# Optimization experiments

Measured on AMD Instinct MI355X. Metric: run time of the kernel, lower is better.

## Reference

```python
import jax, jax.numpy as jnp
import numpy as np

EPS = 1e-5

def channel_norm(x):
    # per-(batch,channel) norm over spatial dims; torch.var default is unbiased (ddof=1)
    mn = x.mean(axis=(-1, -2), keepdims=True)
    std = jnp.sqrt(x.var(axis=(-1, -2), keepdims=True, ddof=1) + EPS)
    return (x - mn) / std

def conv1x1(x, W, b):
    # x: [B,C,H,W], W: [O,C], b: [O]
    return jnp.einsum('oc,bchw->bohw', W, x) + b[None, :, None, None]

def setup_inputs() -> dict:
    key = jax.random.key(0)
    ks = jax.random.split(key, 10)
    B, C, H, W = 4, 512, 64, 64
    s = 1.0 / np.sqrt(C)  # kaiming-uniform-ish scale for 1x1 conv
    inp = {
        'f_c': jax.random.normal(ks[0], (B, C, H, W), jnp.float32),
        'f_s': jax.random.normal(ks[1], (B, C, H, W), jnp.float32),
        'W_c1': jax.random.uniform(ks[2], (C, C), jnp.float32, -s, s),
        'b_c1': jax.random.uniform(ks[3], (C,), jnp.float32, -s, s),
        'W_s1': jax.random.uniform(ks[4], (C, C), jnp.float32, -s, s),
        'b_s1': jax.random.uniform(ks[5], (C,), jnp.float32, -s, s),
        'W_s2': jax.random.uniform(ks[6], (C, C), jnp.float32, -s, s),
        'b_s2': jax.random.uniform(ks[7], (C,), jnp.float32, -s, s),
        'W_csc': jax.random.uniform(ks[8], (C, C), jnp.float32, -s, s),
        'b_csc': jax.random.uniform(ks[9], (C,), jnp.float32, -s, s),
    }
    return inp

def reference(f_c, f_s, W_c1, b_c1, W_s1, b_s1, W_s2, b_s2, W_csc, b_csc):
    B, C, H, W = f_c.shape
    f_c_hat = channel_norm(f_c)
    f_s_hat = channel_norm(f_s)
    f = conv1x1(f_c_hat, W_c1, b_c1).reshape(B, C, H * W)  # queries [B,C,N]
    g = conv1x1(f_s_hat, W_s1, b_s1).reshape(B, C, H * W)  # keys    [B,C,N]
    scores = jnp.einsum('bci,bcj->bij', f, g)              # [B,N,N]
    attention = jax.nn.softmax(scores, axis=-1)
    h = conv1x1(f_s_hat, W_s2, b_s2).reshape(B, C, H * W)  # values  [B,C,N]
    out = jnp.einsum('bcj,bij->bci', h, attention).reshape(B, C, H, W)
    return conv1x1(out, W_csc, b_csc) + f_c
```

## Files before the change

### kernel.cpp

```cpp
#include <hip/hip_runtime.h>

typedef unsigned short u16;
typedef __attribute__((ext_vector_type(8))) _Float16 f16x8;
typedef __attribute__((ext_vector_type(4))) float f32x4;

#define N_SP 4096
#define C_CH 512
#define B_SZ 4

struct PtrTab { u16* p[4]; };

__device__ __forceinline__ u16 f2h(float f) {
    _Float16 h = (_Float16)f;
    union { _Float16 h; u16 u; } x; x.h = h; return x.u;
}
__device__ __forceinline__ float h2f(u16 u) {
    union { u16 u; _Float16 h; } x; x.u = u; return (float)x.h;
}
__device__ __forceinline__ void async_cp16(const void* g, void* l) {
    __builtin_amdgcn_global_load_lds((const __attribute__((address_space(1))) unsigned*)g,
                                     (__attribute__((address_space(3))) unsigned*)l, 16, 0, 0);
}

__device__ __forceinline__ float wave_reduce_sum(float v) {
    #pragma unroll
    for (int off = 32; off; off >>= 1) v += __shfl_xor(v, off, 64);
    return v;
}
__device__ __forceinline__ float wave_reduce_max(float v) {
    #pragma unroll
    for (int off = 32; off; off >>= 1) v = fmaxf(v, __shfl_xor(v, off, 64));
    return v;
}

__global__ __launch_bounds__(256) void stats_kernel(const float* __restrict__ fc,
                                                    const float* __restrict__ fs,
                                                    float* __restrict__ stats) {
    const int idx = blockIdx.x;
    const float* src = (idx < 2048 ? fc : fs) + (size_t)(idx & 2047) * N_SP;
    const int t = threadIdx.x;
    float s = 0.f, ss = 0.f;
    #pragma unroll
    for (int i = 0; i < 4; ++i) {
        float4 v = *(const float4*)(src + i * 1024 + t * 4);
        s  += v.x + v.y + v.z + v.w;
        ss += v.x * v.x + v.y * v.y + v.z * v.z + v.w * v.w;
    }
    s = wave_reduce_sum(s); ss = wave_reduce_sum(ss);
    __shared__ float rs[4], rss[4];
    const int wave = t >> 6;
    if ((t & 63) == 0) { rs[wave] = s; rss[wave] = ss; }
    __syncthreads();
    if (t == 0) {
        const float S  = rs[0] + rs[1] + rs[2] + rs[3];
        const float SS = rss[0] + rss[1] + rss[2] + rss[3];
        const float mean = S * (1.f / N_SP);
        const float var  = (SS - S * mean) * (1.f / (N_SP - 1));
        stats[idx * 2 + 0] = mean;
        stats[idx * 2 + 1] = rsqrtf(var + 1e-5f);
    }
}

__global__ __launch_bounds__(256) void norm_transpose(
        const float* __restrict__ fc, const float* __restrict__ fs,
        const float* __restrict__ stats,
        u16* __restrict__ xc, u16* __restrict__ xs) {
    __shared__ float tile[64][65];
    __shared__ float mi[64][2];
    const int t = threadIdx.x;
    const int n0 = blockIdx.x * 64, c0 = blockIdx.y * 64;
    const int z = blockIdx.z;
    const int b = z & 3, which = z >> 2;
    const float* src = which ? fs : fc;
    u16* dst = which ? xs : xc;
    const float* st = stats + ((size_t)which * 2048 + b * 512 + c0) * 2;
    if (t < 128) ((float*)mi)[t] = st[t];
    __syncthreads();
    const int r = t >> 4, q4 = (t & 15) * 4;
    #pragma unroll
    for (int it = 0; it < 4; ++it) {
        const int row = it * 16 + r;
        float4 v = *(const float4*)(src + ((size_t)b * C_CH + c0 + row) * N_SP + n0 + q4);
        const float mean = mi[row][0], inv = mi[row][1];
        tile[row][q4 + 0] = (v.x - mean) * inv;
        tile[row][q4 + 1] = (v.y - mean) * inv;
        tile[row][q4 + 2] = (v.z - mean) * inv;
        tile[row][q4 + 3] = (v.w - mean) * inv;
    }
    __syncthreads();
    #pragma unroll
    for (int it = 0; it < 4; ++it) {
        const int nrow = it * 16 + r;
        ushort4 h4;
        h4.x = f2h(tile[q4 + 0][nrow]);
        h4.y = f2h(tile[q4 + 1][nrow]);
        h4.z = f2h(tile[q4 + 2][nrow]);
        h4.w = f2h(tile[q4 + 3][nrow]);
        *(ushort4*)(dst + ((size_t)b * N_SP + n0 + nrow) * C_CH + c0 + q4) = h4;
    }
}

__global__ __launch_bounds__(256) void wconv(const float* __restrict__ W0, const float* __restrict__ W1,
                                             const float* __restrict__ W2, const float* __restrict__ W3,
                                             u16* __restrict__ dst) {
    const int i = blockIdx.x * 256 + threadIdx.x;
    const int w = i >> 18, r = i & 262143;
    const float* W = (w == 0) ? W0 : (w == 1) ? W1 : (w == 2) ? W2 : W3;
    dst[i] = f2h(W[r]);
}

enum { OUT_F32 = 0, OUT_F16 = 1 };

template<int OUTMODE, bool TABA, bool TABD>
__global__ __launch_bounds__(256) void gemm_bt(
    const u16* __restrict__ A, const u16* __restrict__ B, PtrTab tab,
    float* __restrict__ Df, u16* __restrict__ Dh,
    const float* __restrict__ bias_m, const float* __restrict__ bias_n,
    const float* __restrict__ res,
    int M, int N, int K, int lda, int ldb, int ldd,
    size_t sA, size_t sB, size_t sD, size_t sR)
{
    constexpr int TM = 128, TN = 128, BK = 32;
    __shared__ u16 smem[(TM + TN) * BK];
    u16* As = smem;
    u16* Bs = smem + TM * BK;

    const int t = threadIdx.x;
    const int l = t & 63, w = t >> 6;
    const int m0 = blockIdx.y * TM, n0 = blockIdx.x * TN;
    const size_t zb = blockIdx.z;
    const u16* pA = (TABA ? tab.p[zb] : A + zb * sA) + (size_t)m0 * lda;
    const u16* pB = B + zb * sB + (size_t)n0 * ldb;

    const int wr = (w & 1) * 64, wc = (w >> 1) * 64;

    f32x4 acc[4][4] = {};

    for (int k0 = 0; k0 < K; k0 += BK) {
        #pragma unroll
        for (int it = 0; it < 2; ++it) {
            const int L = it * 256 + t;
            const int row = L >> 2, cb = (L & 3) * 8;
            async_cp16(pA + (size_t)row * lda + k0 + cb, As + L * 8);
        }
        #pragma unroll
        for (int it = 0; it < 2; ++it) {
            const int L = it * 256 + t;
            const int row = L >> 2, cb = (L & 3) * 8;
            async_cp16(pB + (size_t)row * ldb + k0 + cb, Bs + L * 8);
        }
        __syncthreads();
        f16x8 af[4], bf[4];
        #pragma unroll
        for (int i = 0; i < 4; ++i)
            af[i] = *(const f16x8*)(As + (wr + i * 16 + (l & 15)) * BK + (l >> 4) * 8);
        #pragma unroll
        for (int j = 0; j < 4; ++j)
            bf[j] = *(const f16x8*)(Bs + (wc + j * 16 + (l & 15)) * BK + (l >> 4) * 8);
        #pragma unroll
        for (int i = 0; i < 4; ++i)
            #pragma unroll
            for (int j = 0; j < 4; ++j)
                acc[i][j] = __builtin_amdgcn_mfma_f32_16x16x32_f16(af[i], bf[j], acc[i][j], 0, 0, 0);
        __syncthreads();
    }

    const int em = m0 + wr + (l >> 4) * 4;
    const int en = n0 + wc + (l & 15);
    u16* pDh = nullptr; float* pDf = nullptr;
    if (OUTMODE == OUT_F16) pDh = (TABD ? tab.p[zb] : Dh + zb * sD);
    else                    pDf = Df + zb * sD;
    #pragma unroll
    for (int i = 0; i < 4; ++i) {
        #pragma unroll
        for (int j = 0; j < 4; ++j) {
            const int nn = en + j * 16;
            const float bn = bias_n ? bias_n[nn] : 0.f;
            #pragma unroll
            for (int r = 0; r < 4; ++r) {
                const int mm = em + i * 16 + r;
                float v = acc[i][j][r] + bn;
                if (bias_m) v += bias_m[mm];
                const size_t off = (size_t)mm * ldd + nn;
                if (OUTMODE == OUT_F32) {
                    if (res) v += res[zb * sR + off];
                    pDf[off] = v;
                } else {
                    pDh[off] = f2h(v);
                }
            }
        }
    }
}

__global__ __launch_bounds__(256) void softmax_kernel(PtrTab tab) {
    u16* row = tab.p[blockIdx.y] + (size_t)blockIdx.x * N_SP;
    const int t = threadIdx.x;
    u16 raw[16];
    *(uint4*)(raw + 0) = *(const uint4*)(row + t * 16);
    *(uint4*)(raw + 8) = *(const uint4*)(row + t * 16 + 8);
    float v[16];
    float mx = -1e30f;
    #pragma unroll
    for (int i = 0; i < 16; ++i) { v[i] = h2f(raw[i]); mx = fmaxf(mx, v[i]); }
    mx = wave_reduce_max(mx);
    __shared__ float red[4];
    const int wave = t >> 6;
    if ((t & 63) == 0) red[wave] = mx;
    __syncthreads();
    mx = fmaxf(fmaxf(red[0], red[1]), fmaxf(red[2], red[3]));
    float sum = 0.f;
    #pragma unroll
    for (int i = 0; i < 16; ++i) { v[i] = __expf(v[i] - mx); sum += v[i]; }
    sum = wave_reduce_sum(sum);
    __syncthreads();
    if ((t & 63) == 0) red[wave] = sum;
    __syncthreads();
    const float inv = 1.f / (red[0] + red[1] + red[2] + red[3]);
    #pragma unroll
    for (int i = 0; i < 16; ++i) raw[i] = f2h(v[i] * inv);
    *(uint4*)(row + t * 16)     = *(const uint4*)(raw + 0);
    *(uint4*)(row + t * 16 + 8) = *(const uint4*)(raw + 8);
}

extern "C" void kernel_launch(void* const* d_in, const int* in_sizes, int n_in,
                              void* d_out, int out_size, void* d_ws, size_t ws_size,
                              hipStream_t stream) {
    const float* f_c   = (const float*)d_in[0];
    const float* f_s   = (const float*)d_in[1];
    const float* W_c1  = (const float*)d_in[2];
    const float* b_c1  = (const float*)d_in[3];
    const float* W_s1  = (const float*)d_in[4];
    const float* b_s1  = (const float*)d_in[5];
    const float* W_s2  = (const float*)d_in[6];
    const float* b_s2  = (const float*)d_in[7];
    const float* W_csc = (const float*)d_in[8];
    const float* b_csc = (const float*)d_in[9];

    const size_t PB = (size_t)N_SP * C_CH;
    const size_t M1 = 1024 * 1024;

    u16* ws  = (u16*)d_ws;
    u16* xc  = ws;
    u16* xs  = ws + 8  * M1;
    u16* f_  = ws + 16 * M1;
    u16* g_  = ws + 24 * M1;
    u16* h_  = ws + 32 * M1;
    u16* S1  = ws + 40 * M1;
    u16* S2  = ws + 56 * M1;
    u16* S3  = ws + 72 * M1;
    u16* Wq  = ws + 88 * M1;
    float* stats = (float*)(ws + 89 * M1);
    u16* O_  = f_;
    u16* Wc1 = Wq, *Ws1 = Wq + 262144, *Ws2 = Wq + 524288, *Wcs = Wq + 786432;

    PtrTab Stab; Stab.p[0] = xc; Stab.p[1] = S1; Stab.p[2] = S2; Stab.p[3] = S3;
    PtrTab tab0 = Stab;

    stats_kernel<<<4096, 256, 0, stream>>>(f_c, f_s, stats);
    norm_transpose<<<dim3(64, 8, 8), 256, 0, stream>>>(f_c, f_s, stats, xc, xs);
    wconv<<<4096, 256, 0, stream>>>(W_c1, W_s1, W_s2, W_csc, Wq);

    gemm_bt<OUT_F16, false, false><<<dim3(4, 32, B_SZ), 256, 0, stream>>>(
        xc, Wc1, tab0, nullptr, f_, nullptr, b_c1, nullptr,
        N_SP, C_CH, C_CH, C_CH, C_CH, C_CH, PB, 0, PB, 0);
    gemm_bt<OUT_F16, false, false><<<dim3(4, 32, B_SZ), 256, 0, stream>>>(
        xs, Ws1, tab0, nullptr, g_, nullptr, b_s1, nullptr,
        N_SP, C_CH, C_CH, C_CH, C_CH, C_CH, PB, 0, PB, 0);
    gemm_bt<OUT_F16, false, false><<<dim3(32, 4, B_SZ), 256, 0, stream>>>(
        Ws2, xs, tab0, nullptr, h_, b_s2, nullptr, nullptr,
        C_CH, N_SP, C_CH, C_CH, C_CH, N_SP, 0, PB, PB, 0);

    gemm_bt<OUT_F16, false, true><<<dim3(32, 32, B_SZ), 256, 0, stream>>>(
        f_, g_, Stab, nullptr, nullptr, nullptr, nullptr, nullptr,
        N_SP, N_SP, C_CH, C_CH, C_CH, N_SP, PB, PB, 0, 0);

    softmax_kernel<<<dim3(N_SP, B_SZ), 256, 0, stream>>>(Stab);

    gemm_bt<OUT_F16, true, false><<<dim3(4, 32, B_SZ), 256, 0, stream>>>(
        nullptr, h_, Stab, nullptr, O_, nullptr, nullptr, nullptr,
        N_SP, C_CH, N_SP, N_SP, N_SP, C_CH, 0, PB, PB, 0);

    gemm_bt<OUT_F32, false, false><<<dim3(32, 4, B_SZ), 256, 0, stream>>>(
        Wcs, O_, tab0, (float*)d_out, nullptr, b_csc, nullptr, f_c,
        C_CH, N_SP, C_CH, C_CH, C_CH, N_SP, 0, PB, PB, PB);
}
```

Measured before the change: 521.4 us.

## Fold 1x1 conv weights into attention GEMMs and fuse stats into transpose

Precomputes Ws1^T·Wc1 so queries are projected directly against the normalized style features, which removes the separate key projection. The query-bias term becomes a per-column score bias u, and the softmax-invariant row bias is dropped. It also folds Wcsc into the value projection (Wcsc·Ws2, with a folded bias), so the attention-times-values GEMM writes the final fp32 output plus residual directly and the separate output conv is gone. Stats are now accumulated with atomics during the transpose and normalization is applied afterwards on the fp16 copy, and attention runs in two batch pairs to reuse one score buffer. Costs include extra fp16 rounding from the weight products and from normalizing after the fp16 cast, plus several small extra launches.

```diff
diff --git a/kernel.cpp b/kernel.cpp
--- a/kernel.cpp
+++ b/kernel.cpp
@@ -8,11 +8,8 @@
 #define C_CH 512
 #define B_SZ 4
 
-struct PtrTab { u16* p[4]; };
-
 __device__ __forceinline__ u16 f2h(float f) {
-    _Float16 h = (_Float16)f;
-    union { _Float16 h; u16 u; } x; x.h = h; return x.u;
+    union { _Float16 h; u16 u; } x; x.h = (_Float16)f; return x.u;
 }
 __device__ __forceinline__ float h2f(u16 u) {
     union { u16 u; _Float16 h; } x; x.u = u; return (float)x.h;
@@ -21,7 +18,6 @@
     __builtin_amdgcn_global_load_lds((const __attribute__((address_space(1))) unsigned*)g,
                                      (__attribute__((address_space(3))) unsigned*)l, 16, 0, 0);
 }
-
 __device__ __forceinline__ float wave_reduce_sum(float v) {
     #pragma unroll
     for (int off = 32; off; off >>= 1) v += __shfl_xor(v, off, 64);
@@ -33,61 +29,41 @@
     return v;
 }
 
-__global__ __launch_bounds__(256) void stats_kernel(const float* __restrict__ fc,
-                                                    const float* __restrict__ fs,
-                                                    float* __restrict__ stats) {
-    const int idx = blockIdx.x;
-    const float* src = (idx < 2048 ? fc : fs) + (size_t)(idx & 2047) * N_SP;
-    const int t = threadIdx.x;
-    float s = 0.f, ss = 0.f;
-    #pragma unroll
-    for (int i = 0; i < 4; ++i) {
-        float4 v = *(const float4*)(src + i * 1024 + t * 4);
-        s  += v.x + v.y + v.z + v.w;
-        ss += v.x * v.x + v.y * v.y + v.z * v.z + v.w * v.w;
-    }
-    s = wave_reduce_sum(s); ss = wave_reduce_sum(ss);
-    __shared__ float rs[4], rss[4];
-    const int wave = t >> 6;
-    if ((t & 63) == 0) { rs[wave] = s; rss[wave] = ss; }
-    __syncthreads();
-    if (t == 0) {
-        const float S  = rs[0] + rs[1] + rs[2] + rs[3];
-        const float SS = rss[0] + rss[1] + rss[2] + rss[3];
-        const float mean = S * (1.f / N_SP);
-        const float var  = (SS - S * mean) * (1.f / (N_SP - 1));
-        stats[idx * 2 + 0] = mean;
-        stats[idx * 2 + 1] = rsqrtf(var + 1e-5f);
-    }
-}
-
-__global__ __launch_bounds__(256) void norm_transpose(
+__global__ __launch_bounds__(256) void transpose_cast_stats(
         const float* __restrict__ fc, const float* __restrict__ fs,
-        const float* __restrict__ stats,
-        u16* __restrict__ xc, u16* __restrict__ xs) {
+        u16* __restrict__ xc, u16* __restrict__ xs,
+        float* __restrict__ part_s, float* __restrict__ part_ss) {
     __shared__ float tile[64][65];
-    __shared__ float mi[64][2];
     const int t = threadIdx.x;
     const int n0 = blockIdx.x * 64, c0 = blockIdx.y * 64;
     const int z = blockIdx.z;
     const int b = z & 3, which = z >> 2;
     const float* src = which ? fs : fc;
     u16* dst = which ? xs : xc;
-    const float* st = stats + ((size_t)which * 2048 + b * 512 + c0) * 2;
-    if (t < 128) ((float*)mi)[t] = st[t];
-    __syncthreads();
     const int r = t >> 4, q4 = (t & 15) * 4;
     #pragma unroll
     for (int it = 0; it < 4; ++it) {
         const int row = it * 16 + r;
         float4 v = *(const float4*)(src + ((size_t)b * C_CH + c0 + row) * N_SP + n0 + q4);
-        const float mean = mi[row][0], inv = mi[row][1];
-        tile[row][q4 + 0] = (v.x - mean) * inv;
-        tile[row][q4 + 1] = (v.y - mean) * inv;
-        tile[row][q4 + 2] = (v.z - mean) * inv;
-        tile[row][q4 + 3] = (v.w - mean) * inv;
-    }
-    __syncthreads();
+        tile[row][q4 + 0] = v.x; tile[row][q4 + 1] = v.y;
+        tile[row][q4 + 2] = v.z; tile[row][q4 + 3] = v.w;
+    }
+    __syncthreads();
+    {
+        const int cr = t >> 2, q = t & 3;
+        float s = 0.f, ss = 0.f;
+        #pragma unroll
+        for (int i = 0; i < 16; ++i) {
+            float a = tile[cr][q * 16 + i];
+            s += a; ss += a * a;
+        }
+        s += __shfl_xor(s, 1, 64);  s += __shfl_xor(s, 2, 64);
+        ss += __shfl_xor(ss, 1, 64); ss += __shfl_xor(ss, 2, 64);
+        if (q == 0) {
+            atomicAdd(&part_s[z * 512 + c0 + cr], s);
+            atomicAdd(&part_ss[z * 512 + c0 + cr], ss);
+        }
+    }
     #pragma unroll
     for (int it = 0; it < 4; ++it) {
         const int nrow = it * 16 + r;
@@ -100,27 +76,134 @@
     }
 }
 
-__global__ __launch_bounds__(256) void wconv(const float* __restrict__ W0, const float* __restrict__ W1,
-                                             const float* __restrict__ W2, const float* __restrict__ W3,
-                                             u16* __restrict__ dst) {
-    const int i = blockIdx.x * 256 + threadIdx.x;
-    const int w = i >> 18, r = i & 262143;
-    const float* W = (w == 0) ? W0 : (w == 1) ? W1 : (w == 2) ? W2 : W3;
-    dst[i] = f2h(W[r]);
+__global__ __launch_bounds__(256) void finalize_stats(const float* __restrict__ part_s,
+                                                      const float* __restrict__ part_ss,
+                                                      float* __restrict__ mu_a,
+                                                      float* __restrict__ rs_a) {
+    const int wb = blockIdx.x, t = threadIdx.x;
+    #pragma unroll
+    for (int h = 0; h < 2; ++h) {
+        const int c = wb * 512 + h * 256 + t;
+        const float S = part_s[c], SS = part_ss[c];
+        const float mean = S * (1.f / N_SP);
+        const float var = (SS - S * mean) * (1.f / (N_SP - 1));
+        mu_a[c] = mean;
+        rs_a[c] = rsqrtf(var + 1e-5f);
+    }
+}
+
+__global__ __launch_bounds__(256) void normalize16(u16* __restrict__ xc, u16* __restrict__ xs,
+                                                   const float* __restrict__ mu_a,
+                                                   const float* __restrict__ rs_a) {
+    const int z = blockIdx.y;
+    const int b = z & 3, which = z >> 2;
+    u16* X = (which ? xs : xc) + (size_t)b * (N_SP * C_CH);
+    const size_t e = ((size_t)blockIdx.x * 256 + threadIdx.x) * 8;
+    const int c = (int)(e & 511);
+    u16 v[8];
+    *(uint4*)v = *(const uint4*)(X + e);
+    const float4 mu0 = *(const float4*)(mu_a + z * 512 + c);
+    const float4 mu1 = *(const float4*)(mu_a + z * 512 + c + 4);
+    const float4 rs0 = *(const float4*)(rs_a + z * 512 + c);
+    const float4 rs1 = *(const float4*)(rs_a + z * 512 + c + 4);
+    const float mu[8] = {mu0.x, mu0.y, mu0.z, mu0.w, mu1.x, mu1.y, mu1.z, mu1.w};
+    const float rs[8] = {rs0.x, rs0.y, rs0.z, rs0.w, rs1.x, rs1.y, rs1.z, rs1.w};
+    #pragma unroll
+    for (int i = 0; i < 8; ++i) v[i] = f2h((h2f(v[i]) - mu[i]) * rs[i]);
+    *(uint4*)(X + e) = *(const uint4*)v;
+}
+
+__global__ __launch_bounds__(256) void wtrans(const float* __restrict__ W0, const float* __restrict__ W1,
+                                              const float* __restrict__ W2, const float* __restrict__ W3,
+                                              u16* __restrict__ D0, u16* __restrict__ D1,
+                                              u16* __restrict__ D2, u16* __restrict__ D3) {
+    __shared__ float tile[64][65];
+    const int t = threadIdx.x, z = blockIdx.z;
+    const int n0 = blockIdx.x * 64, c0 = blockIdx.y * 64;
+    const float* W = (z == 0) ? W0 : (z == 1) ? W1 : (z == 2) ? W2 : W3;
+    u16* D = (z == 0) ? D0 : (z == 1) ? D1 : (z == 2) ? D2 : D3;
+    const int r = t >> 4, q4 = (t & 15) * 4;
+    #pragma unroll
+    for (int it = 0; it < 4; ++it) {
+        const int row = it * 16 + r;
+        float4 v = *(const float4*)(W + (size_t)(c0 + row) * 512 + n0 + q4);
+        if (z == 3) {
+            ushort4 h4 = { f2h(v.x), f2h(v.y), f2h(v.z), f2h(v.w) };
+            *(ushort4*)(D + (size_t)(c0 + row) * 512 + n0 + q4) = h4;
+        } else {
+            tile[row][q4 + 0] = v.x; tile[row][q4 + 1] = v.y;
+            tile[row][q4 + 2] = v.z; tile[row][q4 + 3] = v.w;
+        }
+    }
+    __syncthreads();
+    if (z == 3) return;
+    #pragma unroll
+    for (int it = 0; it < 4; ++it) {
+        const int nrow = it * 16 + r;
+        ushort4 h4;
+        h4.x = f2h(tile[q4 + 0][nrow]);
+        h4.y = f2h(tile[q4 + 1][nrow]);
+        h4.z = f2h(tile[q4 + 2][nrow]);
+        h4.w = f2h(tile[q4 + 3][nrow]);
+        *(ushort4*)(D + (size_t)(n0 + nrow) * 512 + c0 + q4) = h4;
+    }
+}
+
+__global__ __launch_bounds__(256) void wu_gemv(const float* __restrict__ Ws1,
+                                               const float* __restrict__ bc1,
+                                               float* __restrict__ w_u) {
+    const int d = blockIdx.x * 256 + threadIdx.x;
+    float acc = 0.f;
+    for (int o = 0; o < 512; ++o) acc += bc1[o] * Ws1[(size_t)o * 512 + d];
+    w_u[d] = acc;
+}
+
+__global__ __launch_bounds__(256) void bfold_gemv(const float* __restrict__ Wcsc,
+                                                  const float* __restrict__ bs2,
+                                                  const float* __restrict__ bcsc,
+                                                  float* __restrict__ bfold0) {
+    const int o = blockIdx.x * 4 + (threadIdx.x >> 6), l = threadIdx.x & 63;
+    const float4 w0 = *(const float4*)(Wcsc + (size_t)o * 512 + l * 8);
+    const float4 w1 = *(const float4*)(Wcsc + (size_t)o * 512 + l * 8 + 4);
+    const float4 b0 = *(const float4*)(bs2 + l * 8);
+    const float4 b1 = *(const float4*)(bs2 + l * 8 + 4);
+    float acc = w0.x * b0.x + w0.y * b0.y + w0.z * b0.z + w0.w * b0.w
+              + w1.x * b1.x + w1.y * b1.y + w1.z * b1.z + w1.w * b1.w;
+    acc = wave_reduce_sum(acc);
+    if (l == 0) bfold0[o] = acc + bcsc[o];
+}
+
+__global__ __launch_bounds__(256) void u_big(const u16* __restrict__ xs,
+                                             const float* __restrict__ w_u,
+                                             float* __restrict__ u) {
+    const int b = blockIdx.y, w = threadIdx.x >> 6, l = threadIdx.x & 63;
+    const float4 u0 = *(const float4*)(w_u + l * 8);
+    const float4 u1 = *(const float4*)(w_u + l * 8 + 4);
+    #pragma unroll
+    for (int jj = 0; jj < 16; ++jj) {
+        const int j = blockIdx.x * 64 + w * 16 + jj;
+        const u16* row = xs + ((size_t)b * N_SP + j) * C_CH + l * 8;
+        f16x8 x = *(const f16x8*)row;
+        float acc = (float)x[0] * u0.x + (float)x[1] * u0.y + (float)x[2] * u0.z + (float)x[3] * u0.w
+                  + (float)x[4] * u1.x + (float)x[5] * u1.y + (float)x[6] * u1.z + (float)x[7] * u1.w;
+        acc = wave_reduce_sum(acc);
+        if (l == 0) u[(size_t)b * N_SP + j] = acc;
+    }
 }
 
 enum { OUT_F32 = 0, OUT_F16 = 1 };
 
-template<int OUTMODE, bool TABA, bool TABD>
+template<int OUTMODE, int TM>
 __global__ __launch_bounds__(256) void gemm_bt(
-    const u16* __restrict__ A, const u16* __restrict__ B, PtrTab tab,
+    const u16* __restrict__ A, const u16* __restrict__ B,
     float* __restrict__ Df, u16* __restrict__ Dh,
     const float* __restrict__ bias_m, const float* __restrict__ bias_n,
     const float* __restrict__ res,
     int M, int N, int K, int lda, int ldb, int ldd,
-    size_t sA, size_t sB, size_t sD, size_t sR)
+    size_t sA, size_t sB, size_t sD, size_t sR, int sBm, int sBn)
 {
-    constexpr int TM = 128, TN = 128, BK = 32;
+    constexpr int TN = 128, BK = 32;
+    constexpr int FM = TM / 32;
     __shared__ u16 smem[(TM + TN) * BK];
     u16* As = smem;
     u16* Bs = smem + TM * BK;
@@ -129,16 +212,16 @@
     const int l = t & 63, w = t >> 6;
     const int m0 = blockIdx.y * TM, n0 = blockIdx.x * TN;
     const size_t zb = blockIdx.z;
-    const u16* pA = (TABA ? tab.p[zb] : A + zb * sA) + (size_t)m0 * lda;
+    const u16* pA = A + zb * sA + (size_t)m0 * lda;
     const u16* pB = B + zb * sB + (size_t)n0 * ldb;
 
-    const int wr = (w & 1) * 64, wc = (w >> 1) * 64;
-
-    f32x4 acc[4][4] = {};
+    const int wr = (w & 1) * (TM / 2), wc = (w >> 1) * 64;
+
+    f32x4 acc[FM][4] = {};
 
     for (int k0 = 0; k0 < K; k0 += BK) {
         #pragma unroll
-        for (int it = 0; it < 2; ++it) {
+        for (int it = 0; it < TM / 64; ++it) {
             const int L = it * 256 + t;
             const int row = L >> 2, cb = (L & 3) * 8;
             async_cp16(pA + (size_t)row * lda + k0 + cb, As + L * 8);
@@ -150,15 +233,15 @@
             async_cp16(pB + (size_t)row * ldb + k0 + cb, Bs + L * 8);
         }
         __syncthreads();
-        f16x8 af[4], bf[4];
-        #pragma unroll
-        for (int i = 0; i < 4; ++i)
+        f16x8 af[FM], bf[4];
+        #pragma unroll
+        for (int i = 0; i < FM; ++i)
             af[i] = *(const f16x8*)(As + (wr + i * 16 + (l & 15)) * BK + (l >> 4) * 8);
         #pragma unroll
         for (int j = 0; j < 4; ++j)
             bf[j] = *(const f16x8*)(Bs + (wc + j * 16 + (l & 15)) * BK + (l >> 4) * 8);
         #pragma unroll
-        for (int i = 0; i < 4; ++i)
+        for (int i = 0; i < FM; ++i)
             #pragma unroll
             for (int j = 0; j < 4; ++j)
                 acc[i][j] = __builtin_amdgcn_mfma_f32_16x16x32_f16(af[i], bf[j], acc[i][j], 0, 0, 0);
@@ -167,20 +250,19 @@
 
     const int em = m0 + wr + (l >> 4) * 4;
     const int en = n0 + wc + (l & 15);
-    u16* pDh = nullptr; float* pDf = nullptr;
-    if (OUTMODE == OUT_F16) pDh = (TABD ? tab.p[zb] : Dh + zb * sD);
-    else                    pDf = Df + zb * sD;
-    #pragma unroll
-    for (int i = 0; i < 4; ++i) {
+    u16* pDh = (OUTMODE == OUT_F16) ? (Dh + zb * sD) : nullptr;
+    float* pDf = (OUTMODE == OUT_F32) ? (Df + zb * sD) : nullptr;
+    #pragma unroll
+    for (int i = 0; i < FM; ++i) {
         #pragma unroll
         for (int j = 0; j < 4; ++j) {
             const int nn = en + j * 16;
-            const float bn = bias_n ? bias_n[nn] : 0.f;
+            const float bn = bias_n ? bias_n[(size_t)sBn * zb + nn] : 0.f;
             #pragma unroll
             for (int r = 0; r < 4; ++r) {
                 const int mm = em + i * 16 + r;
                 float v = acc[i][j][r] + bn;
-                if (bias_m) v += bias_m[mm];
+                if (bias_m) v += bias_m[(size_t)sBm * zb + mm];
                 const size_t off = (size_t)mm * ldd + nn;
                 if (OUTMODE == OUT_F32) {
                     if (res) v += res[zb * sR + off];
@@ -193,8 +275,8 @@
     }
 }
 
-__global__ __launch_bounds__(256) void softmax_kernel(PtrTab tab) {
-    u16* row = tab.p[blockIdx.y] + (size_t)blockIdx.x * N_SP;
+__global__ __launch_bounds__(256) void softmax_kernel(u16* __restrict__ Sbase, size_t sS) {
+    u16* row = Sbase + blockIdx.y * sS + (size_t)blockIdx.x * N_SP;
     const int t = threadIdx.x;
     u16 raw[16];
     *(uint4*)(raw + 0) = *(const uint4*)(row + t * 16);
@@ -231,7 +313,7 @@
     const float* W_c1  = (const float*)d_in[2];
     const float* b_c1  = (const float*)d_in[3];
     const float* W_s1  = (const float*)d_in[4];
-    const float* b_s1  = (const float*)d_in[5];
+    const float* b_s1  = (const float*)d_in[5]; (void)b_s1;
     const float* W_s2  = (const float*)d_in[6];
     const float* b_s2  = (const float*)d_in[7];
     const float* W_csc = (const float*)d_in[8];
@@ -239,49 +321,62 @@
 
     const size_t PB = (size_t)N_SP * C_CH;
     const size_t M1 = 1024 * 1024;
-
-    u16* ws  = (u16*)d_ws;
-    u16* xc  = ws;
-    u16* xs  = ws + 8  * M1;
-    u16* f_  = ws + 16 * M1;
-    u16* g_  = ws + 24 * M1;
-    u16* h_  = ws + 32 * M1;
-    u16* S1  = ws + 40 * M1;
-    u16* S2  = ws + 56 * M1;
-    u16* S3  = ws + 72 * M1;
-    u16* Wq  = ws + 88 * M1;
-    float* stats = (float*)(ws + 89 * M1);
-    u16* O_  = f_;
-    u16* Wc1 = Wq, *Ws1 = Wq + 262144, *Ws2 = Wq + 524288, *Wcs = Wq + 786432;
-
-    PtrTab Stab; Stab.p[0] = xc; Stab.p[1] = S1; Stab.p[2] = S2; Stab.p[3] = S3;
-    PtrTab tab0 = Stab;
-
-    stats_kernel<<<4096, 256, 0, stream>>>(f_c, f_s, stats);
-    norm_transpose<<<dim3(64, 8, 8), 256, 0, stream>>>(f_c, f_s, stats, xc, xs);
-    wconv<<<4096, 256, 0, stream>>>(W_c1, W_s1, W_s2, W_csc, Wq);
-
-    gemm_bt<OUT_F16, false, false><<<dim3(4, 32, B_SZ), 256, 0, stream>>>(
-        xc, Wc1, tab0, nullptr, f_, nullptr, b_c1, nullptr,
-        N_SP, C_CH, C_CH, C_CH, C_CH, C_CH, PB, 0, PB, 0);
-    gemm_bt<OUT_F16, false, false><<<dim3(4, 32, B_SZ), 256, 0, stream>>>(
-        xs, Ws1, tab0, nullptr, g_, nullptr, b_s1, nullptr,
-        N_SP, C_CH, C_CH, C_CH, C_CH, C_CH, PB, 0, PB, 0);
-    gemm_bt<OUT_F16, false, false><<<dim3(32, 4, B_SZ), 256, 0, stream>>>(
-        Ws2, xs, tab0, nullptr, h_, b_s2, nullptr, nullptr,
-        C_CH, N_SP, C_CH, C_CH, C_CH, N_SP, 0, PB, PB, 0);
-
-    gemm_bt<OUT_F16, false, true><<<dim3(32, 32, B_SZ), 256, 0, stream>>>(
-        f_, g_, Stab, nullptr, nullptr, nullptr, nullptr, nullptr,
-        N_SP, N_SP, C_CH, C_CH, C_CH, N_SP, PB, PB, 0, 0);
-
-    softmax_kernel<<<dim3(N_SP, B_SZ), 256, 0, stream>>>(Stab);
-
-    gemm_bt<OUT_F16, true, false><<<dim3(4, 32, B_SZ), 256, 0, stream>>>(
-        nullptr, h_, Stab, nullptr, O_, nullptr, nullptr, nullptr,
-        N_SP, C_CH, N_SP, N_SP, N_SP, C_CH, 0, PB, PB, 0);
-
-    gemm_bt<OUT_F32, false, false><<<dim3(32, 4, B_SZ), 256, 0, stream>>>(
-        Wcs, O_, tab0, (float*)d_out, nullptr, b_csc, nullptr, f_c,
-        C_CH, N_SP, C_CH, C_CH, C_CH, N_SP, 0, PB, PB, PB);
-}
+    const size_t SSTR = 16 * M1;
+
+    u16* ws   = (u16*)d_ws;
+    u16* Xc   = ws;
+    u16* Xs   = ws + 8 * M1;
+    u16* q_   = ws + 16 * M1;
+    u16* hc   = ws + 24 * M1;
+    u16* S0   = ws + 32 * M1;
+    u16* Wc1T = ws + 64 * M1;
+    u16* Ws1T = Wc1T + 262144;
+    u16* Ws2T = Ws1T + 262144;
+    u16* Wcs16= Ws2T + 262144;
+    u16* WqT  = ws + 65 * M1;
+    u16* Wf16 = WqT + 262144;
+    float* f32b = (float*)(ws + 66 * M1);
+    float* part_s  = f32b;
+    float* part_ss = f32b + 4096;
+    float* mu_a    = f32b + 8192;
+    float* rs_a    = f32b + 12288;
+    float* w_u     = f32b + 16384;
+    float* bfold0  = f32b + 16896;
+    float* u_      = f32b + 17408;
+
+    hipMemsetAsync(part_s, 0, 2 * 4096 * sizeof(float), stream);
+
+    transpose_cast_stats<<<dim3(64, 8, 8), 256, 0, stream>>>(f_c, f_s, Xc, Xs, part_s, part_ss);
+    finalize_stats<<<8, 256, 0, stream>>>(part_s, part_ss, mu_a, rs_a);
+    normalize16<<<dim3(1024, 8), 256, 0, stream>>>(Xc, Xs, mu_a, rs_a);
+
+    wtrans<<<dim3(8, 8, 4), 256, 0, stream>>>(W_c1, W_s1, W_s2, W_csc, Wc1T, Ws1T, Ws2T, Wcs16);
+    wu_gemv<<<2, 256, 0, stream>>>(W_s1, b_c1, w_u);
+    bfold_gemv<<<128, 256, 0, stream>>>(W_csc, b_s2, b_csc, bfold0);
+
+    gemm_bt<OUT_F16, 128><<<dim3(4, 4, 1), 256, 0, stream>>>(
+        Ws1T, Wc1T, nullptr, WqT, nullptr, nullptr, nullptr,
+        512, 512, 512, 512, 512, 512, 0, 0, 0, 0, 0, 0);
+    gemm_bt<OUT_F16, 128><<<dim3(4, 4, 1), 256, 0, stream>>>(
+        Wcs16, Ws2T, nullptr, Wf16, nullptr, nullptr, nullptr,
+        512, 512, 512, 512, 512, 512, 0, 0, 0, 0, 0, 0);
+
+    gemm_bt<OUT_F16, 128><<<dim3(4, 32, B_SZ), 256, 0, stream>>>(
+        Xc, WqT, nullptr, q_, nullptr, nullptr, nullptr,
+        N_SP, C_CH, C_CH, C_CH, C_CH, C_CH, PB, 0, PB, 0, 0, 0);
+    gemm_bt<OUT_F16, 128><<<dim3(32, 4, B_SZ), 256, 0, stream>>>(
+        Wf16, Xs, nullptr, hc, bfold0, nullptr, nullptr,
+        C_CH, N_SP, C_CH, C_CH, C_CH, N_SP, 0, PB, PB, 0, 0, 0);
+    u_big<<<dim3(64, B_SZ), 256, 0, stream>>>(Xs, w_u, u_);
+
+    for (int g = 0; g < 2; ++g) {
+        gemm_bt<OUT_F16, 128><<<dim3(32, 32, 2), 256, 0, stream>>>(
+            q_ + g * 2 * PB, Xs + g * 2 * PB, nullptr, S0, nullptr, u_ + g * 2 * N_SP, nullptr,
+            N_SP, N_SP, C_CH, C_CH, C_CH, N_SP, PB, PB, SSTR, 0, 0, N_SP);
+        softmax_kernel<<<dim3(N_SP, 2), 256, 0, stream>>>(S0, SSTR);
+        gemm_bt<OUT_F32, 64><<<dim3(32, 8, 2), 256, 0, stream>>>(
+            hc + g * 2 * PB, S0, (float*)d_out + g * 2 * PB, nullptr, nullptr, nullptr,
+            f_c + g * 2 * PB,
+            C_CH, N_SP, N_SP, N_SP, N_SP, N_SP, PB, SSTR, PB, PB, 0, 0);
+    }
+}
```

Measured after the change: 584.4 us. 1.12x slower.
